# Kernel tuning notes

Hardware: AMD Instinct MI355X
Metric: run time of the kernel (lower is better)

The kernel has to match this reference:

```python
import jax, jax.numpy as jnp
import numpy as np

HIDDEN = 768
NUM_HEADS = 12
HEAD_DIM = HIDDEN // NUM_HEADS  # 64
BATCH = 1
SEQ = 4096


def setup_inputs() -> dict:
    key = jax.random.key(0)
    ks = jax.random.split(key, 10)
    s = 0.02
    return {
        "hidden_states": jax.random.normal(ks[0], (BATCH, SEQ, HIDDEN), dtype=jnp.float32),
        "attention_mask": jnp.zeros((BATCH, 1, 1, SEQ), dtype=jnp.float32),
        "q_w": jax.random.normal(ks[1], (HIDDEN, HIDDEN), dtype=jnp.float32) * s,
        "q_b": jnp.zeros((HIDDEN,), dtype=jnp.float32),
        "k_w": jax.random.normal(ks[2], (HIDDEN, HIDDEN), dtype=jnp.float32) * s,
        "k_b": jnp.zeros((HIDDEN,), dtype=jnp.float32),
        "v_w": jax.random.normal(ks[3], (HIDDEN, HIDDEN), dtype=jnp.float32) * s,
        "v_b": jnp.zeros((HIDDEN,), dtype=jnp.float32),
        "out_w": jax.random.normal(ks[4], (HIDDEN, HIDDEN), dtype=jnp.float32) * s,
        "out_b": jnp.zeros((HIDDEN,), dtype=jnp.float32),
    }


def reference(hidden_states, attention_mask, q_w, q_b, k_w, k_b, v_w, v_b, out_w, out_b):
    B, S, _ = hidden_states.shape
    scale = 1.0 / np.sqrt(HEAD_DIM).astype(np.float32)

    def split_heads(x):
        # [B, S, H*D] -> [B, H, S, D]
        return x.reshape(B, S, NUM_HEADS, HEAD_DIM).transpose(0, 2, 1, 3)

    q = split_heads(hidden_states @ q_w.T + q_b)
    k = split_heads(hidden_states @ k_w.T + k_b)
    v = split_heads(hidden_states @ v_w.T + v_b)

    # [B, H, S, S] score tensor (materialized, as in the original module)
    scores = jnp.einsum("bhqd,bhkd->bhqk", q, k) * scale + attention_mask
    probs = jax.nn.softmax(scores, axis=-1)
    ctx = jnp.einsum("bhqk,bhkd->bhqd", probs, v)
    ctx = ctx.transpose(0, 2, 1, 3).reshape(B, S, HIDDEN)
    return ctx @ out_w.T + out_b
```

## Files before the change

kernel.cpp:

```cpp
#include <hip/hip_runtime.h>
#include <hip/hip_bf16.h>

#define SEQ  4096
#define HID  768
#define NH   12
#define HD   64
#define QKVN 2304
#define KVB  32
#define SPLIT 4
#define NT   ((SEQ/SPLIT)/KVB)

typedef __attribute__((ext_vector_type(8)))  short  short8;
typedef __attribute__((ext_vector_type(4)))  float  f32x4;
typedef __attribute__((ext_vector_type(16))) float  f32x16;

static __device__ __forceinline__ unsigned short bf16b(float x) {
  __hip_bfloat16 h = __float2bfloat16(x);
  return *reinterpret_cast<unsigned short*>(&h);
}
static __device__ __forceinline__ unsigned pkbf(float lo, float hi) {
  return (unsigned)bf16b(lo) | ((unsigned)bf16b(hi) << 16);
}
static __device__ __forceinline__ void store4(__hip_bfloat16* p, float a, float b, float c, float d) {
  unsigned long long v = (unsigned long long)pkbf(a, b) | ((unsigned long long)pkbf(c, d) << 32);
  *reinterpret_cast<unsigned long long*>(p) = v;
}
static __device__ __forceinline__ void gload16(const void* g, void* l) {
  __builtin_amdgcn_global_load_lds(
      (const __attribute__((address_space(1))) void*)g,
      (__attribute__((address_space(3))) void*)l, 16, 0, 0);
}

static __device__ __forceinline__ void cvt_store(float* p, float v) { *p = v; }
static __device__ __forceinline__ void cvt_store(__hip_bfloat16* p, float v) { *p = __float2bfloat16(v); }

__global__ __launch_bounds__(256) void prep_kernel(
    const float* __restrict__ hs,
    const float* __restrict__ qw, const float* __restrict__ kw,
    const float* __restrict__ vw, const float* __restrict__ ow,
    const float* __restrict__ qb, const float* __restrict__ kb,
    const float* __restrict__ vb,
    __hip_bfloat16* __restrict__ Xb,
    __hip_bfloat16* __restrict__ Wqkv,
    __hip_bfloat16* __restrict__ Wo,
    float* __restrict__ bqkv)
{
  const int NX = SEQ*HID/4, NW = QKVN*HID/4, NO = HID*HID/4, NB = QKVN/4;
  int idx = blockIdx.x*256 + threadIdx.x;
  if (idx < NX) {
    float4 v = ((const float4*)hs)[idx];
    store4(Xb + idx*4, v.x, v.y, v.z, v.w);
  } else if (idx < NX + NW) {
    int f = (idx - NX)*4;
    int row = f / HID, col = f - row*HID;
    const float* src = (row < HID)   ? qw + row*HID + col
                     : (row < 2*HID) ? kw + (row-HID)*HID + col
                     :                 vw + (row-2*HID)*HID + col;
    float4 v = *(const float4*)src;
    store4(Wqkv + f, v.x, v.y, v.z, v.w);
  } else if (idx < NX + NW + NO) {
    int li = idx - NX - NW;
    float4 v = ((const float4*)ow)[li];
    store4(Wo + li*4, v.x, v.y, v.z, v.w);
  } else if (idx < NX + NW + NO + NB) {
    int f = (idx - NX - NW - NO)*4;
    const float* src = (f < HID) ? qb + f : (f < 2*HID) ? kb + (f-HID) : vb + (f-2*HID);
    *(float4*)(bqkv + f) = *(const float4*)src;
  }
}

template <typename OutT>
__global__ __launch_bounds__(256) void gemm_nt(
    const __hip_bfloat16* __restrict__ A,
    const __hip_bfloat16* __restrict__ B,
    const float* __restrict__ bias,
    OutT* __restrict__ C, int N, int K)
{
  __shared__ __align__(16) short As[128*32];
  __shared__ __align__(16) short Bs[128*32];
  const int tid  = threadIdx.x;
  const int lane = tid & 63;
  const int w    = tid >> 6;
  const int m0   = blockIdx.y * 128;
  const int n0   = blockIdx.x * 128;
  const int wrow = w >> 1, wcol = w & 1;
  const int l15  = lane & 15;
  const int k8   = (lane >> 4) * 8;

  f32x4 acc[4][4] = {};

  const int base0 = w*512;
  const int base1 = (4+w)*512;
  const int f0 = base0 + lane*8, f1 = base1 + lane*8;
  const __hip_bfloat16* Ap0 = A + (long)(m0 + (f0>>5))*K + (f0&31);
  const __hip_bfloat16* Ap1 = A + (long)(m0 + (f1>>5))*K + (f1&31);
  const __hip_bfloat16* Bp0 = B + (long)(n0 + (f0>>5))*K + (f0&31);
  const __hip_bfloat16* Bp1 = B + (long)(n0 + (f1>>5))*K + (f1&31);

  for (int k0 = 0; k0 < K; k0 += 32) {
    gload16(Ap0 + k0, As + base0);
    gload16(Ap1 + k0, As + base1);
    gload16(Bp0 + k0, Bs + base0);
    gload16(Bp1 + k0, Bs + base1);
    __syncthreads();

    short8 af[4], bfm[4];
#pragma unroll
    for (int mi = 0; mi < 4; ++mi)
      af[mi] = *(const short8*)&As[(wrow*64 + mi*16 + l15)*32 + k8];
#pragma unroll
    for (int ni = 0; ni < 4; ++ni)
      bfm[ni] = *(const short8*)&Bs[(wcol*64 + ni*16 + l15)*32 + k8];
#pragma unroll
    for (int mi = 0; mi < 4; ++mi)
#pragma unroll
      for (int ni = 0; ni < 4; ++ni)
        acc[mi][ni] = __builtin_amdgcn_mfma_f32_16x16x32_bf16(af[mi], bfm[ni], acc[mi][ni], 0, 0, 0);
    __syncthreads();
  }

  const int rbase = (lane >> 4) * 4;
#pragma unroll
  for (int mi = 0; mi < 4; ++mi)
#pragma unroll
    for (int ni = 0; ni < 4; ++ni) {
      int gm = m0 + wrow*64 + mi*16 + rbase;
      int gn = n0 + wcol*64 + ni*16 + l15;
      float bv = bias[gn];
#pragma unroll
      for (int r = 0; r < 4; ++r)
        cvt_store(&C[(long)(gm + r)*N + gn], acc[mi][ni][r] + bv);
    }
}

__global__ __launch_bounds__(128, 4) void attn_fwd(
    const __hip_bfloat16* __restrict__ QKV,
    const float* __restrict__ mask,
    float* __restrict__ Oacc,
    float* __restrict__ Lacc)
{
  __shared__ __align__(16) char SMEM[18432];
  short* KsB = (short*)SMEM;
  short* VTB = (short*)(SMEM + 8192);
  float* Of  = (float*)SMEM;

  const int tid  = threadIdx.x;
  const int lane = tid & 63;
  const int wv   = tid >> 6;
  const int head = blockIdx.y;
  const int qt   = blockIdx.x;
  const int s0   = blockIdx.z * (SEQ/SPLIT);
  const int q0   = qt*64 + wv*32;
  const int ql   = lane & 31;
  const int hi   = lane >> 5;
  const float scale = 0.125f;

  short8 qf[4];
  {
    const __hip_bfloat16* qrow = QKV + (long)(q0+ql)*QKVN + head*HD + hi*8;
#pragma unroll
    for (int dc = 0; dc < 4; ++dc)
      qf[dc] = *(const short8*)(qrow + dc*16);
  }

  const __hip_bfloat16* kp[2];
#pragma unroll
  for (int i = 0; i < 2; ++i) {
    int slot = i*128 + tid;
    int krow = slot >> 3, kcs = slot & 7;
    kp[i] = QKV + (long)(s0 + krow)*QKVN + HID + head*HD + ((kcs ^ (krow & 7))*8);
  }

  const int vkv2 = (tid & 15)*2, vdb = (tid >> 4)*8;
  const __hip_bfloat16* vsrc = QKV + (long)(s0 + vkv2)*QKVN + 2*HID + head*HD + vdb;

  f32x16 oacc[2] = {};
  float lrun = 0.0f;

  short8 va = *(const short8*)(vsrc);
  short8 vb = *(const short8*)(vsrc + QKVN);
  {
    short* vt = VTB;
#pragma unroll
    for (int e = 0; e < 8; ++e) {
      unsigned w0 = (unsigned)(unsigned short)va[e] | ((unsigned)(unsigned short)vb[e] << 16);
      *(unsigned*)&vt[(vdb + e)*40 + vkv2] = w0;
    }
#pragma unroll
    for (int i = 0; i < 2; ++i)
      gload16(kp[i], KsB + (i*128 + wv*64)*8);
    const __hip_bfloat16* pv = vsrc + (long)KVB*QKVN;
    va = *(const short8*)(pv);
    vb = *(const short8*)(pv + QKVN);
  }
  __syncthreads();

  for (int t = 0; t < NT; ++t) {
    const int cur = t & 1, nxt = cur ^ 1;
    short* ksC = KsB + cur*2048;
    short* vtC = VTB + cur*2560;
    {
      short* vtN = VTB + nxt*2560;
#pragma unroll
      for (int e = 0; e < 8; ++e) {
        unsigned w0 = (unsigned)(unsigned short)va[e] | ((unsigned)(unsigned short)vb[e] << 16);
        *(unsigned*)&vtN[(vdb + e)*40 + vkv2] = w0;
      }
      const long kn = (long)(((t+1) < NT) ? (t+1) : t) * KVB * QKVN;
      short* ksN = KsB + nxt*2048;
#pragma unroll
      for (int i = 0; i < 2; ++i)
        gload16(kp[i] + kn, ksN + (i*128 + wv*64)*8);
      const long kn2 = (long)(((t+2) < NT) ? (t+2) : (NT-1)) * KVB * QKVN;
      va = *(const short8*)(vsrc + kn2);
      vb = *(const short8*)(vsrc + kn2 + QKVN);
    }
    const float* mrow = mask + s0 + t*KVB;
    float4 mg[4];
#pragma unroll
    for (int g = 0; g < 4; ++g)
      mg[g] = *(const float4*)(mrow + 8*g + 4*hi);

    short8 kf[4];
#pragma unroll
    for (int dc = 0; dc < 4; ++dc)
      kf[dc] = *(const short8*)&ksC[ql*64 + (((dc*2 + hi) ^ (ql & 7))*8)];
    f32x16 sacc = {};
#pragma unroll
    for (int dc = 0; dc < 4; ++dc)
      sacc = __builtin_amdgcn_mfma_f32_32x32x16_bf16(kf[dc], qf[dc], sacc, 0, 0, 0);

    float p[16];
#pragma unroll
    for (int g = 0; g < 4; ++g) {
      p[4*g+0] = __expf(sacc[4*g+0]*scale + mg[g].x);
      p[4*g+1] = __expf(sacc[4*g+1]*scale + mg[g].y);
      p[4*g+2] = __expf(sacc[4*g+2]*scale + mg[g].z);
      p[4*g+3] = __expf(sacc[4*g+3]*scale + mg[g].w);
    }
    float sl0 = 0.f, sl1 = 0.f;
#pragma unroll
    for (int r = 0; r < 8; ++r) { sl0 += p[r]; sl1 += p[8+r]; }
    lrun += sl0 + sl1;

    unsigned pk[8], pr[8];
#pragma unroll
    for (int u = 0; u < 8; ++u) pk[u] = pkbf(p[2*u], p[2*u+1]);
#pragma unroll
    for (int u = 0; u < 8; ++u) pr[u] = (unsigned)__shfl_xor((int)pk[u], 32);
    unsigned b0[4], b1[4];
    b0[0] = hi ? pr[2] : pk[0];  b0[1] = hi ? pr[3] : pk[1];
    b0[2] = hi ? pk[2] : pr[0];  b0[3] = hi ? pk[3] : pr[1];
    b1[0] = hi ? pr[6] : pk[4];  b1[1] = hi ? pr[7] : pk[5];
    b1[2] = hi ? pk[6] : pr[4];  b1[3] = hi ? pk[7] : pr[5];
    union U { unsigned u[4]; short8 s; };
    U pb0{{b0[0], b0[1], b0[2], b0[3]}};
    U pb1{{b1[0], b1[1], b1[2], b1[3]}};

    short8 a00 = *(const short8*)&vtC[(ql)*40      + hi*8];
    short8 a01 = *(const short8*)&vtC[(ql)*40 + 16 + hi*8];
    short8 a10 = *(const short8*)&vtC[(32+ql)*40      + hi*8];
    short8 a11 = *(const short8*)&vtC[(32+ql)*40 + 16 + hi*8];

    oacc[0] = __builtin_amdgcn_mfma_f32_32x32x16_bf16(a00, pb0.s, oacc[0], 0, 0, 0);
    oacc[0] = __builtin_amdgcn_mfma_f32_32x32x16_bf16(a01, pb1.s, oacc[0], 0, 0, 0);
    oacc[1] = __builtin_amdgcn_mfma_f32_32x32x16_bf16(a10, pb0.s, oacc[1], 0, 0, 0);
    oacc[1] = __builtin_amdgcn_mfma_f32_32x32x16_bf16(a11, pb1.s, oacc[1], 0, 0, 0);
    __syncthreads();
  }

  float lp = lrun + __shfl_xor(lrun, 32);
  if (hi == 0)
    unsafeAtomicAdd(&Lacc[head*SEQ + q0 + ql], lp);

#pragma unroll
  for (int cb = 0; cb < 2; ++cb)
#pragma unroll
    for (int g = 0; g < 4; ++g)
#pragma unroll
      for (int r = 0; r < 4; ++r)
        Of[(wv*32 + ql)*65 + cb*32 + 8*g + 4*hi + r] = oacc[cb][4*g + r];
  __syncthreads();

  const int qbase = qt*64;
  float* orow = Oacc + (long)qbase*HID + head*HD + lane;
#pragma unroll 4
  for (int r = 0; r < 32; ++r) {
    int q = wv*32 + r;
    unsafeAtomicAdd(orow + (long)q*HID, Of[q*65 + lane]);
  }
}

__global__ __launch_bounds__(256) void finalize_kernel(
    const float* __restrict__ Oacc, const float* __restrict__ Lacc,
    __hip_bfloat16* __restrict__ ctx)
{
  int idx = blockIdx.x*256 + threadIdx.x;
  int q  = idx / (HID/4);
  int c4 = (idx - q*(HID/4))*4;
  float inv = 1.0f / Lacc[(c4 >> 6)*SEQ + q];
  float4 o = *(const float4*)&Oacc[(long)q*HID + c4];
  store4(ctx + (long)q*HID + c4, o.x*inv, o.y*inv, o.z*inv, o.w*inv);
}

extern "C" void kernel_launch(void* const* d_in, const int* in_sizes, int n_in,
                              void* d_out, int out_size, void* d_ws, size_t ws_size,
                              hipStream_t stream) {
  const float* hs  = (const float*)d_in[0];
  const float* msk = (const float*)d_in[1];
  const float* qw  = (const float*)d_in[2];
  const float* qb  = (const float*)d_in[3];
  const float* kw  = (const float*)d_in[4];
  const float* kb  = (const float*)d_in[5];
  const float* vw  = (const float*)d_in[6];
  const float* vb  = (const float*)d_in[7];
  const float* ow  = (const float*)d_in[8];
  const float* ob  = (const float*)d_in[9];

  char* ws = (char*)d_ws;
  __hip_bfloat16* Xb   = (__hip_bfloat16*)(ws);
  __hip_bfloat16* Wqkv = (__hip_bfloat16*)(ws + 6291456);
  __hip_bfloat16* Wo   = (__hip_bfloat16*)(ws + 9830400);
  float*          bqkv = (float*)         (ws + 11010048);
  __hip_bfloat16* QKV  = (__hip_bfloat16*)(ws + 11019264);
  __hip_bfloat16* Ctx  = (__hip_bfloat16*)(ws + 29893632);
  float*          Oacc = (float*)         (ws + 36185088);
  float*          Lacc = (float*)         (ws + 48768000);

  hipMemsetAsync(Oacc, 0, 12582912 + 196608, stream);

  {
    const int total = SEQ*HID/4 + QKVN*HID/4 + HID*HID/4 + QKVN/4;
    prep_kernel<<<(total + 255)/256, 256, 0, stream>>>(hs, qw, kw, vw, ow, qb, kb, vb,
                                                       Xb, Wqkv, Wo, bqkv);
  }
  gemm_nt<__hip_bfloat16><<<dim3(QKVN/128, SEQ/128), 256, 0, stream>>>(Xb, Wqkv, bqkv, QKV, QKVN, HID);
  attn_fwd<<<dim3(SEQ/64, NH, SPLIT), 128, 0, stream>>>(QKV, msk, Oacc, Lacc);
  finalize_kernel<<<(SEQ*HID/4)/256, 256, 0, stream>>>(Oacc, Lacc, Ctx);
  gemm_nt<float><<<dim3(HID/128, SEQ/128), 256, 0, stream>>>(Ctx, Wo, ob, (float*)d_out, HID, HID);
}
```

Before: 189.2 us.

## Widen attention blocks to four waves sharing K/V tiles, use exp2 and permlane swap

The attention kernel now runs 256-thread blocks covering 128 queries, so each K/V tile loaded into LDS is shared by four waves instead of two, and each thread loads half as much. Softmax switches to exp2, with log2e folded into the score scale and into a pre-scaled mask produced by the prep kernel. The cross-half P shuffle uses permlane32_swap where the builtin exists. The output reduction is staged in two phases through the same LDS buffer. The grid has half as many blocks, and the larger blocks with a higher launch-bounds occupancy hint may add register pressure.

After: 273.2 us. +44.4%, slower.

```diff
diff --git a/kernel.cpp b/kernel.cpp
--- a/kernel.cpp
+++ b/kernel.cpp
@@ -9,8 +9,10 @@
 #define KVB  32
 #define SPLIT 4
 #define NT   ((SEQ/SPLIT)/KVB)
+#define LOG2E 1.44269504f
 
 typedef __attribute__((ext_vector_type(8)))  short  short8;
+typedef __attribute__((ext_vector_type(4)))  short  s16x4;
 typedef __attribute__((ext_vector_type(4)))  float  f32x4;
 typedef __attribute__((ext_vector_type(16))) float  f32x16;
 
@@ -29,6 +31,25 @@
   __builtin_amdgcn_global_load_lds(
       (const __attribute__((address_space(1))) void*)g,
       (__attribute__((address_space(3))) void*)l, 16, 0, 0);
+}
+
+#if __has_builtin(__builtin_amdgcn_exp2f)
+#define EXP2(x) __builtin_amdgcn_exp2f(x)
+#else
+#define EXP2(x) __expf((x) * 0.6931472f)
+#endif
+
+static __device__ __forceinline__ void swap32(unsigned a, unsigned b, unsigned& x, unsigned& y) {
+#if __has_builtin(__builtin_amdgcn_permlane32_swap)
+  auto r = __builtin_amdgcn_permlane32_swap((int)a, (int)b, false, false);
+  x = (unsigned)r[0]; y = (unsigned)r[1];
+#else
+  unsigned pa = (unsigned)__shfl_xor((int)a, 32);
+  unsigned pb = (unsigned)__shfl_xor((int)b, 32);
+  int hi = (int)((threadIdx.x & 63) >> 5);
+  x = hi ? pb : a;
+  y = hi ? b : pa;
+#endif
 }
 
 static __device__ __forceinline__ void cvt_store(float* p, float v) { *p = v; }
@@ -39,13 +60,14 @@
     const float* __restrict__ qw, const float* __restrict__ kw,
     const float* __restrict__ vw, const float* __restrict__ ow,
     const float* __restrict__ qb, const float* __restrict__ kb,
-    const float* __restrict__ vb,
+    const float* __restrict__ vb, const float* __restrict__ msk,
     __hip_bfloat16* __restrict__ Xb,
     __hip_bfloat16* __restrict__ Wqkv,
     __hip_bfloat16* __restrict__ Wo,
-    float* __restrict__ bqkv)
+    float* __restrict__ bqkv,
+    float* __restrict__ mask2)
 {
-  const int NX = SEQ*HID/4, NW = QKVN*HID/4, NO = HID*HID/4, NB = QKVN/4;
+  const int NX = SEQ*HID/4, NW = QKVN*HID/4, NO = HID*HID/4, NB = QKVN/4, NM = SEQ/4;
   int idx = blockIdx.x*256 + threadIdx.x;
   if (idx < NX) {
     float4 v = ((const float4*)hs)[idx];
@@ -66,6 +88,11 @@
     int f = (idx - NX - NW - NO)*4;
     const float* src = (f < HID) ? qb + f : (f < 2*HID) ? kb + (f-HID) : vb + (f-2*HID);
     *(float4*)(bqkv + f) = *(const float4*)src;
+  } else if (idx < NX + NW + NO + NB + NM) {
+    int f = (idx - NX - NW - NO - NB)*4;
+    float4 v = *(const float4*)(msk + f);
+    float4 o; o.x = v.x*LOG2E; o.y = v.y*LOG2E; o.z = v.z*LOG2E; o.w = v.w*LOG2E;
+    *(float4*)(mask2 + f) = o;
   }
 }
 
@@ -133,9 +160,9 @@
     }
 }
 
-__global__ __launch_bounds__(128, 4) void attn_fwd(
+__global__ __launch_bounds__(256, 6) void attn_fwd(
     const __hip_bfloat16* __restrict__ QKV,
-    const float* __restrict__ mask,
+    const float* __restrict__ mask2,
     float* __restrict__ Oacc,
     float* __restrict__ Lacc)
 {
@@ -150,10 +177,10 @@
   const int head = blockIdx.y;
   const int qt   = blockIdx.x;
   const int s0   = blockIdx.z * (SEQ/SPLIT);
-  const int q0   = qt*64 + wv*32;
+  const int q0   = qt*128 + wv*32;
   const int ql   = lane & 31;
   const int hi   = lane >> 5;
-  const float scale = 0.125f;
+  const float scale2 = 0.125f * LOG2E;
 
   short8 qf[4];
   {
@@ -163,35 +190,31 @@
       qf[dc] = *(const short8*)(qrow + dc*16);
   }
 
-  const __hip_bfloat16* kp[2];
-#pragma unroll
-  for (int i = 0; i < 2; ++i) {
-    int slot = i*128 + tid;
+  const __hip_bfloat16* kp;
+  {
+    int slot = wv*64 + lane;
     int krow = slot >> 3, kcs = slot & 7;
-    kp[i] = QKV + (long)(s0 + krow)*QKVN + HID + head*HD + ((kcs ^ (krow & 7))*8);
-  }
-
-  const int vkv2 = (tid & 15)*2, vdb = (tid >> 4)*8;
-  const __hip_bfloat16* vsrc = QKV + (long)(s0 + vkv2)*QKVN + 2*HID + head*HD + vdb;
+    kp = QKV + (long)(s0 + krow)*QKVN + HID + head*HD + ((kcs ^ (krow & 7))*8);
+  }
+
+  const int vkv2 = (tid & 15)*2, vdb4 = (tid >> 4)*4;
+  const __hip_bfloat16* vsrc = QKV + (long)(s0 + vkv2)*QKVN + 2*HID + head*HD + vdb4;
 
   f32x16 oacc[2] = {};
   float lrun = 0.0f;
 
-  short8 va = *(const short8*)(vsrc);
-  short8 vb = *(const short8*)(vsrc + QKVN);
+  s16x4 va = *(const s16x4*)(vsrc);
+  s16x4 vb = *(const s16x4*)(vsrc + QKVN);
   {
-    short* vt = VTB;
-#pragma unroll
-    for (int e = 0; e < 8; ++e) {
+#pragma unroll
+    for (int e = 0; e < 4; ++e) {
       unsigned w0 = (unsigned)(unsigned short)va[e] | ((unsigned)(unsigned short)vb[e] << 16);
-      *(unsigned*)&vt[(vdb + e)*40 + vkv2] = w0;
-    }
-#pragma unroll
-    for (int i = 0; i < 2; ++i)
-      gload16(kp[i], KsB + (i*128 + wv*64)*8);
+      *(unsigned*)&VTB[(vdb4 + e)*40 + vkv2] = w0;
+    }
+    gload16(kp, KsB + wv*64*8);
     const __hip_bfloat16* pv = vsrc + (long)KVB*QKVN;
-    va = *(const short8*)(pv);
-    vb = *(const short8*)(pv + QKVN);
+    va = *(const s16x4*)(pv);
+    vb = *(const s16x4*)(pv + QKVN);
   }
   __syncthreads();
 
@@ -202,20 +225,17 @@
     {
       short* vtN = VTB + nxt*2560;
 #pragma unroll
-      for (int e = 0; e < 8; ++e) {
+      for (int e = 0; e < 4; ++e) {
         unsigned w0 = (unsigned)(unsigned short)va[e] | ((unsigned)(unsigned short)vb[e] << 16);
-        *(unsigned*)&vtN[(vdb + e)*40 + vkv2] = w0;
+        *(unsigned*)&vtN[(vdb4 + e)*40 + vkv2] = w0;
       }
       const long kn = (long)(((t+1) < NT) ? (t+1) : t) * KVB * QKVN;
-      short* ksN = KsB + nxt*2048;
-#pragma unroll
-      for (int i = 0; i < 2; ++i)
-        gload16(kp[i] + kn, ksN + (i*128 + wv*64)*8);
+      gload16(kp + kn, KsB + nxt*2048 + wv*64*8);
       const long kn2 = (long)(((t+2) < NT) ? (t+2) : (NT-1)) * KVB * QKVN;
-      va = *(const short8*)(vsrc + kn2);
-      vb = *(const short8*)(vsrc + kn2 + QKVN);
-    }
-    const float* mrow = mask + s0 + t*KVB;
+      va = *(const s16x4*)(vsrc + kn2);
+      vb = *(const s16x4*)(vsrc + kn2 + QKVN);
+    }
+    const float* mrow = mask2 + s0 + t*KVB;
     float4 mg[4];
 #pragma unroll
     for (int g = 0; g < 4; ++g)
@@ -233,26 +253,24 @@
     float p[16];
 #pragma unroll
     for (int g = 0; g < 4; ++g) {
-      p[4*g+0] = __expf(sacc[4*g+0]*scale + mg[g].x);
-      p[4*g+1] = __expf(sacc[4*g+1]*scale + mg[g].y);
-      p[4*g+2] = __expf(sacc[4*g+2]*scale + mg[g].z);
-      p[4*g+3] = __expf(sacc[4*g+3]*scale + mg[g].w);
+      p[4*g+0] = EXP2(sacc[4*g+0]*scale2 + mg[g].x);
+      p[4*g+1] = EXP2(sacc[4*g+1]*scale2 + mg[g].y);
+      p[4*g+2] = EXP2(sacc[4*g+2]*scale2 + mg[g].z);
+      p[4*g+3] = EXP2(sacc[4*g+3]*scale2 + mg[g].w);
     }
     float sl0 = 0.f, sl1 = 0.f;
 #pragma unroll
     for (int r = 0; r < 8; ++r) { sl0 += p[r]; sl1 += p[8+r]; }
     lrun += sl0 + sl1;
 
-    unsigned pk[8], pr[8];
+    unsigned pk[8];
 #pragma unroll
     for (int u = 0; u < 8; ++u) pk[u] = pkbf(p[2*u], p[2*u+1]);
-#pragma unroll
-    for (int u = 0; u < 8; ++u) pr[u] = (unsigned)__shfl_xor((int)pk[u], 32);
     unsigned b0[4], b1[4];
-    b0[0] = hi ? pr[2] : pk[0];  b0[1] = hi ? pr[3] : pk[1];
-    b0[2] = hi ? pk[2] : pr[0];  b0[3] = hi ? pk[3] : pr[1];
-    b1[0] = hi ? pr[6] : pk[4];  b1[1] = hi ? pr[7] : pk[5];
-    b1[2] = hi ? pk[6] : pr[4];  b1[3] = hi ? pk[7] : pr[5];
+    swap32(pk[0], pk[2], b0[0], b0[2]);
+    swap32(pk[1], pk[3], b0[1], b0[3]);
+    swap32(pk[4], pk[6], b1[0], b1[2]);
+    swap32(pk[5], pk[7], b1[1], b1[3]);
     union U { unsigned u[4]; short8 s; };
     U pb0{{b0[0], b0[1], b0[2], b0[3]}};
     U pb1{{b1[0], b1[1], b1[2], b1[3]}};
@@ -274,20 +292,25 @@
     unsafeAtomicAdd(&Lacc[head*SEQ + q0 + ql], lp);
 
 #pragma unroll
-  for (int cb = 0; cb < 2; ++cb)
-#pragma unroll
-    for (int g = 0; g < 4; ++g)
-#pragma unroll
-      for (int r = 0; r < 4; ++r)
-        Of[(wv*32 + ql)*65 + cb*32 + 8*g + 4*hi + r] = oacc[cb][4*g + r];
-  __syncthreads();
-
-  const int qbase = qt*64;
-  float* orow = Oacc + (long)qbase*HID + head*HD + lane;
+  for (int ph = 0; ph < 2; ++ph) {
+    __syncthreads();
+    if ((wv >> 1) == ph) {
+      int row = (wv & 1)*32 + ql;
+#pragma unroll
+      for (int cb = 0; cb < 2; ++cb)
+#pragma unroll
+        for (int g = 0; g < 4; ++g)
+#pragma unroll
+          for (int r = 0; r < 4; ++r)
+            Of[row*65 + cb*32 + 8*g + 4*hi + r] = oacc[cb][4*g + r];
+    }
+    __syncthreads();
+    float* obase = Oacc + (long)(qt*128 + ph*64)*HID + head*HD + lane;
 #pragma unroll 4
-  for (int r = 0; r < 32; ++r) {
-    int q = wv*32 + r;
-    unsafeAtomicAdd(orow + (long)q*HID, Of[q*65 + lane]);
+    for (int r = 0; r < 16; ++r) {
+      int row = wv*16 + r;
+      unsafeAtomicAdd(obase + (long)row*HID, Of[row*65 + lane]);
+    }
   }
 }
 
@@ -326,16 +349,17 @@
   __hip_bfloat16* Ctx  = (__hip_bfloat16*)(ws + 29893632);
   float*          Oacc = (float*)         (ws + 36185088);
   float*          Lacc = (float*)         (ws + 48768000);
+  float*          Mask2= (float*)         (ws + 48964608);
 
   hipMemsetAsync(Oacc, 0, 12582912 + 196608, stream);
 
   {
-    const int total = SEQ*HID/4 + QKVN*HID/4 + HID*HID/4 + QKVN/4;
-    prep_kernel<<<(total + 255)/256, 256, 0, stream>>>(hs, qw, kw, vw, ow, qb, kb, vb,
-                                                       Xb, Wqkv, Wo, bqkv);
+    const int total = SEQ*HID/4 + QKVN*HID/4 + HID*HID/4 + QKVN/4 + SEQ/4;
+    prep_kernel<<<(total + 255)/256, 256, 0, stream>>>(hs, qw, kw, vw, ow, qb, kb, vb, msk,
+                                                       Xb, Wqkv, Wo, bqkv, Mask2);
   }
   gemm_nt<__hip_bfloat16><<<dim3(QKVN/128, SEQ/128), 256, 0, stream>>>(Xb, Wqkv, bqkv, QKV, QKVN, HID);
-  attn_fwd<<<dim3(SEQ/64, NH, SPLIT), 128, 0, stream>>>(QKV, msk, Oacc, Lacc);
+  attn_fwd<<<dim3(SEQ/128, NH, SPLIT), 256, 0, stream>>>(QKV, Mask2, Oacc, Lacc);
   finalize_kernel<<<(SEQ*HID/4)/256, 256, 0, stream>>>(Oacc, Lacc, Ctx);
   gemm_nt<float><<<dim3(HID/128, SEQ/128), 256, 0, stream>>>(Ctx, Wo, ob, (float*)d_out, HID, HID);
 }
```
